# Kernel optimization log

Measured on AMD Instinct MI355X. Metric: run time of the kernel, lower is better.

The kernel has to match this reference:

```python
import jax, jax.numpy as jnp
import numpy as np

N_NODES = 50000
N_EDGES = 800000
N_GRAPHS = 64
D_IN = 96
D_HID = 96
D_OUT = 2
NEG_SLOPE = 0.2


def setup_inputs() -> dict:
    key = jax.random.key(0)
    ks = jax.random.split(key, 9)
    x = jax.random.normal(ks[0], (N_NODES, D_IN), dtype=jnp.float32)
    edge_index = jax.random.randint(ks[1], (2, N_EDGES), 0, N_NODES, dtype=jnp.int32)
    batch = jnp.sort(jax.random.randint(ks[2], (N_NODES,), 0, N_GRAPHS, dtype=jnp.int32))
    s1 = 1.0 / np.sqrt(D_IN)
    s2 = 1.0 / np.sqrt(D_HID)
    W1 = jax.random.normal(ks[3], (D_IN, D_HID), dtype=jnp.float32) * s1
    b1 = jnp.zeros((D_HID,), dtype=jnp.float32)
    W2 = jax.random.normal(ks[4], (D_HID, D_HID), dtype=jnp.float32) * s2
    b2 = jnp.zeros((D_HID,), dtype=jnp.float32)
    Wc = jax.random.normal(ks[5], (D_HID, D_OUT), dtype=jnp.float32) * s2
    bc = jnp.zeros((D_OUT,), dtype=jnp.float32)
    return {"x": x, "edge_index": edge_index, "batch": batch,
            "W1": W1, "b1": b1, "W2": W2, "b2": b2, "Wc": Wc, "bc": bc}


def _gcn_conv(h, W, b, src, dst, n_nodes):
    # GCNConv (Kipf): add self-loops, symmetric deg^-1/2 normalization.
    hW = h @ W  # [N, F]
    deg = jnp.zeros((n_nodes,), dtype=hW.dtype).at[dst].add(1.0) + 1.0  # +1 self-loop
    dinv = jax.lax.rsqrt(deg)
    coef = (dinv[src] * dinv[dst])[:, None]            # [E, 1]
    agg = jnp.zeros_like(hW).at[dst].add(hW[src] * coef)
    out = agg + hW * (dinv * dinv)[:, None] + b        # self-loop term: deg^-1 * hW
    return out


def _leaky(h):
    return jnp.where(h > 0, h, NEG_SLOPE * h)


def reference(x, edge_index, batch, W1, b1, W2, b2, Wc, bc):
    src, dst = edge_index[0], edge_index[1]
    h = _leaky(_gcn_conv(x, W1, b1, src, dst, N_NODES))
    h = _leaky(_gcn_conv(h, W2, b2, src, dst, N_NODES))
    # global_mean_pool over graph ids
    sums = jax.ops.segment_sum(h, batch, num_segments=N_GRAPHS)
    cnts = jax.ops.segment_sum(jnp.ones((N_NODES,), dtype=h.dtype), batch, num_segments=N_GRAPHS)
    pooled = sums / jnp.maximum(cnts, 1.0)[:, None]    # [G, F]
    return pooled @ Wc + bc                             # [G, D_OUT]
```

## Files before the change

### kernel.cpp

```cpp
#include <hip/hip_runtime.h>
#include <hip/hip_fp16.h>

#define NN 50000
#define NE 800000
#define NG 64
#define DF 96
#define SLOPE 0.2f
#define NBK 196
#define EB 196
#define PC 12

__global__ __launch_bounds__(256) void k_hist(const int* __restrict__ dst,
                                              int* __restrict__ hist2d) {
  __shared__ int h[NBK];
  int t = threadIdx.x;
  if (t < NBK) h[t] = 0;
  __syncthreads();
  int base = blockIdx.x * 4096;
  for (int k = 0; k < 16; ++k) {
    int e = base + k * 256 + t;
    if (e < NE) atomicAdd(&h[dst[e] >> 8], 1);
  }
  __syncthreads();
  if (t < NBK) hist2d[blockIdx.x * NBK + t] = h[t];
}

__global__ __launch_bounds__(256) void k_colscan(const int* __restrict__ hist2d,
                                                 int* __restrict__ colpref,
                                                 int* __restrict__ coltotal,
                                                 const int* __restrict__ batch,
                                                 int* __restrict__ gstart) {
  __shared__ int s[256];
  int col = blockIdx.x;
  int b = threadIdx.x;
  int v = (b < EB) ? hist2d[b * NBK + col] : 0;
  s[b] = v;
  __syncthreads();
  for (int o = 1; o < 256; o <<= 1) {
    int u = (b >= o) ? s[b - o] : 0;
    __syncthreads();
    s[b] += u;
    __syncthreads();
  }
  if (b < EB) colpref[b * NBK + col] = s[b] - v;
  if (b == 255) coltotal[col] = s[b];
  if (blockIdx.x == 0 && b <= NG) {
    int g = b, lo = 0, hi = NN;
    while (lo < hi) {
      int mid = (lo + hi) >> 1;
      if (batch[mid] < g) lo = mid + 1; else hi = mid;
    }
    gstart[g] = lo;
  }
}

__global__ __launch_bounds__(256) void k_bin2(const int* __restrict__ src,
                                              const int* __restrict__ dst,
                                              const int* __restrict__ hist2d,
                                              const int* __restrict__ coltotal,
                                              const int* __restrict__ colpref,
                                              int* __restrict__ binned) {
  __shared__ int h[NBK], loff[NBK], cur[NBK], gb[NBK];
  __shared__ int tmp[256];
  __shared__ int stage[4096];
  __shared__ unsigned char sbk[4096];
  int t = threadIdx.x;
  int ctv = (t < NBK) ? coltotal[t] : 0;
  tmp[t] = ctv;
  __syncthreads();
  for (int o = 1; o < 256; o <<= 1) {
    int u = (t >= o) ? tmp[t - o] : 0;
    __syncthreads();
    tmp[t] += u;
    __syncthreads();
  }
  int bbase_t = tmp[t] - ctv;
  if (t < NBK) h[t] = hist2d[blockIdx.x * NBK + t];
  __syncthreads();
  tmp[t] = (t < NBK) ? h[t] : 0;
  __syncthreads();
  for (int o = 1; o < 256; o <<= 1) {
    int u = (t >= o) ? tmp[t - o] : 0;
    __syncthreads();
    tmp[t] += u;
    __syncthreads();
  }
  if (t < NBK) {
    int excl = tmp[t] - h[t];
    loff[t] = excl;
    cur[t] = excl;
    gb[t] = bbase_t + colpref[blockIdx.x * NBK + t];
  }
  __syncthreads();
  int base = blockIdx.x * 4096;
  for (int k = 0; k < 16; ++k) {
    int e = base + k * 256 + t;
    if (e < NE) {
      int d = dst[e];
      int b = d >> 8;
      int p = atomicAdd(&cur[b], 1);
      stage[p] = src[e] | ((d & 255) << 16);
      sbk[p] = (unsigned char)b;
    }
  }
  __syncthreads();
  int tot = min(4096, NE - base);
  for (int i = t; i < tot; i += 256) {
    int b = sbk[i];
    binned[gb[b] + (i - loff[b])] = stage[i];
  }
}

__global__ __launch_bounds__(256) void k_csr(const int* __restrict__ binned,
                                             const int* __restrict__ coltotal,
                                             float* __restrict__ dinv,
                                             int* __restrict__ row_start,
                                             unsigned short* __restrict__ csr_src) {
  __shared__ int h[256], cur[256], tmp[256];
  int t = threadIdx.x;
  int b = blockIdx.x;
  int ctv = (t < NBK) ? coltotal[t] : 0;
  h[t] = ctv;
  tmp[t] = ctv;
  __syncthreads();
  for (int o = 1; o < 256; o <<= 1) {
    int u = (t >= o) ? tmp[t - o] : 0;
    __syncthreads();
    tmp[t] += u;
    __syncthreads();
  }
  int ebeg = tmp[b] - h[b];
  int eend = tmp[b];
  __syncthreads();
  h[t] = 0;
  __syncthreads();
  for (int i = ebeg + t; i < eend; i += 256) atomicAdd(&h[(unsigned)binned[i] >> 16], 1);
  __syncthreads();
  tmp[t] = h[t];
  __syncthreads();
  for (int o = 1; o < 256; o <<= 1) {
    int v = (t >= o) ? tmp[t - o] : 0;
    __syncthreads();
    tmp[t] += v;
    __syncthreads();
  }
  int excl = tmp[t] - h[t];
  int rs = ebeg + excl;
  cur[t] = rs;
  int n = b * 256 + t;
  if (n < NN) {
    row_start[n] = rs;
    dinv[n] = rsqrtf((float)h[t] + 1.0f);
  }
  if (b == NBK - 1 && t == 255) row_start[NN] = NE;
  __syncthreads();
  for (int i = ebeg + t; i < eend; i += 256) {
    int pr = binned[i];
    int p = atomicAdd(&cur[(unsigned)pr >> 16], 1);
    csr_src[p] = (unsigned short)(pr & 0xFFFF);
  }
}

#define GR 64
template <typename T>
__global__ __launch_bounds__(256) void k_gemm(const T* __restrict__ X,
                                              const float* __restrict__ W,
                                              const float* __restrict__ dinv,
                                              __half* __restrict__ G) {
  __shared__ float Ws[DF * DF];
  int t = threadIdx.x;
  for (int i = t; i < DF * DF / 4; i += 256)
    ((float4*)Ws)[i] = ((const float4*)W)[i];
  __syncthreads();
  int tc = t & 15;
  int tr = t >> 4;
  int c0 = tc * 6;
  int r0 = blockIdx.x * GR + tr * 4;
  const T* xp[4];
#pragma unroll
  for (int i = 0; i < 4; ++i) xp[i] = X + (size_t)min(r0 + i, NN - 1) * DF;

  float acc[4][6];
#pragma unroll
  for (int i = 0; i < 4; ++i)
#pragma unroll
    for (int j = 0; j < 6; ++j) acc[i][j] = 0.f;

#pragma unroll 4
  for (int k4 = 0; k4 < DF / 4; ++k4) {
    float xr[4][4];
#pragma unroll
    for (int i = 0; i < 4; ++i) {
      if constexpr (sizeof(T) == 4) {
        float4 v = ((const float4*)xp[i])[k4];
        xr[i][0] = v.x; xr[i][1] = v.y; xr[i][2] = v.z; xr[i][3] = v.w;
      } else {
        uint2 hv = ((const uint2*)xp[i])[k4];
        float2 a = __half22float2(*(__half2*)&hv.x);
        float2 b = __half22float2(*(__half2*)&hv.y);
        xr[i][0] = a.x; xr[i][1] = a.y; xr[i][2] = b.x; xr[i][3] = b.y;
      }
    }
#pragma unroll
    for (int kk = 0; kk < 4; ++kk) {
      int k = k4 * 4 + kk;
      float2 w0 = *(float2*)&Ws[k * DF + c0];
      float2 w1 = *(float2*)&Ws[k * DF + c0 + 2];
      float2 w2 = *(float2*)&Ws[k * DF + c0 + 4];
      float wv[6] = {w0.x, w0.y, w1.x, w1.y, w2.x, w2.y};
#pragma unroll
      for (int i = 0; i < 4; ++i)
#pragma unroll
        for (int j = 0; j < 6; ++j) acc[i][j] = fmaf(xr[i][kk], wv[j], acc[i][j]);
    }
  }
#pragma unroll
  for (int i = 0; i < 4; ++i) {
    int row = r0 + i;
    if (row < NN) {
      float dv = dinv[row];
      __half2* gp = (__half2*)(G + (size_t)row * DF + c0);
#pragma unroll
      for (int j = 0; j < 3; ++j)
        gp[j] = __floats2half2_rn(acc[i][2 * j] * dv, acc[i][2 * j + 1] * dv);
    }
  }
}

__global__ __launch_bounds__(256) void k_agg(const __half* __restrict__ G,
                                             const float* __restrict__ dinv,
                                             const float* __restrict__ bias,
                                             const int* __restrict__ row_start,
                                             const unsigned short* __restrict__ csr_src,
                                             __half* __restrict__ H) {
  int lane = threadIdx.x & 15;
  int n = blockIdx.x * 16 + (threadIdx.x >> 4);
  if (n >= NN) return;
  const unsigned* rn = (const unsigned*)(G + (size_t)n * DF);
  unsigned su0 = rn[lane], su1 = rn[lane + 16], su2 = rn[lane + 32];
  float2 f0 = __half22float2(*(__half2*)&su0);
  float2 f1 = __half22float2(*(__half2*)&su1);
  float2 f2 = __half22float2(*(__half2*)&su2);
  float a00 = f0.x, a01 = f0.y, a10 = f1.x, a11 = f1.y, a20 = f2.x, a21 = f2.y;

  int s = row_start[n], e = row_start[n + 1];
  for (int j0 = s; j0 < e; j0 += 16) {
    int my = (j0 + lane < e) ? (int)csr_src[j0 + lane] : 0;
    int cnt = min(16, e - j0);
    int jj = 0;
    for (; jj + 8 <= cnt; jj += 8) {
      unsigned u[8][3];
#pragma unroll
      for (int q = 0; q < 8; ++q) {
        int srcn = __shfl(my, jj + q, 16);
        const unsigned* r2 = (const unsigned*)(G + (size_t)srcn * DF);
        u[q][0] = r2[lane];
        u[q][1] = r2[lane + 16];
        u[q][2] = r2[lane + 32];
      }
#pragma unroll
      for (int q = 0; q < 8; ++q) {
        float2 g0 = __half22float2(*(__half2*)&u[q][0]);
        float2 g1 = __half22float2(*(__half2*)&u[q][1]);
        float2 g2 = __half22float2(*(__half2*)&u[q][2]);
        a00 += g0.x; a01 += g0.y;
        a10 += g1.x; a11 += g1.y;
        a20 += g2.x; a21 += g2.y;
      }
    }
    for (; jj < cnt; ++jj) {
      int srcn = __shfl(my, jj, 16);
      const unsigned* r2 = (const unsigned*)(G + (size_t)srcn * DF);
      unsigned v0 = r2[lane], v1 = r2[lane + 16], v2 = r2[lane + 32];
      float2 g0 = __half22float2(*(__half2*)&v0);
      float2 g1 = __half22float2(*(__half2*)&v1);
      float2 g2 = __half22float2(*(__half2*)&v2);
      a00 += g0.x; a01 += g0.y;
      a10 += g1.x; a11 += g1.y;
      a20 += g2.x; a21 += g2.y;
    }
  }
  float dv = dinv[n];
  float2 b0 = *(const float2*)(bias + 2 * lane);
  float2 b1 = *(const float2*)(bias + 2 * lane + 32);
  float2 b2 = *(const float2*)(bias + 2 * lane + 64);
  float v00 = dv * a00 + b0.x, v01 = dv * a01 + b0.y;
  float v10 = dv * a10 + b1.x, v11 = dv * a11 + b1.y;
  float v20 = dv * a20 + b2.x, v21 = dv * a21 + b2.y;
  v00 = v00 > 0.f ? v00 : SLOPE * v00;
  v01 = v01 > 0.f ? v01 : SLOPE * v01;
  v10 = v10 > 0.f ? v10 : SLOPE * v10;
  v11 = v11 > 0.f ? v11 : SLOPE * v11;
  v20 = v20 > 0.f ? v20 : SLOPE * v20;
  v21 = v21 > 0.f ? v21 : SLOPE * v21;
  __half2* hp = (__half2*)(H + (size_t)n * DF);
  hp[lane] = __floats2half2_rn(v00, v01);
  hp[lane + 16] = __floats2half2_rn(v10, v11);
  hp[lane + 32] = __floats2half2_rn(v20, v21);
}

__global__ __launch_bounds__(384) void k_pool2(const __half* __restrict__ H,
                                               const int* __restrict__ gstart,
                                               float* __restrict__ partial) {
  int g = blockIdx.x / PC, c = blockIdx.x % PC;
  int f2 = threadIdx.x % 48;
  int r = threadIdx.x / 48;
  int s = gstart[g], e = gstart[g + 1];
  int len = (e - s + PC - 1) / PC;
  int cs = s + c * len, ce = min(cs + len, e);
  float ax = 0.f, ay = 0.f;
  for (int n = cs + r; n < ce; n += 8) {
    float2 v = __half22float2(((const __half2*)(H + (size_t)n * DF))[f2]);
    ax += v.x;
    ay += v.y;
  }
  __shared__ float2 red[8][48];
  red[r][f2] = float2{ax, ay};
  __syncthreads();
  if (r == 0) {
    float sx = 0.f, sy = 0.f;
#pragma unroll
    for (int q = 0; q < 8; ++q) { sx += red[q][f2].x; sy += red[q][f2].y; }
    partial[(size_t)blockIdx.x * DF + 2 * f2] = sx;
    partial[(size_t)blockIdx.x * DF + 2 * f2 + 1] = sy;
  }
}

__global__ __launch_bounds__(128) void k_pool3(const float* __restrict__ partial,
                                               const int* __restrict__ gstart,
                                               const float* __restrict__ Wc,
                                               const float* __restrict__ bc,
                                               float* __restrict__ out) {
  __shared__ float pm[DF];
  int g = blockIdx.x;
  int t = threadIdx.x;
  if (t < DF) {
    float s = 0.f;
    for (int c = 0; c < PC; ++c) s += partial[(size_t)(g * PC + c) * DF + t];
    float cnt = (float)(gstart[g + 1] - gstart[g]);
    pm[t] = s / fmaxf(cnt, 1.0f);
  }
  __syncthreads();
  if (t < 2) {
    float s = 0.f;
    for (int c = 0; c < DF; ++c) s += pm[c] * Wc[c * 2 + t];
    out[g * 2 + t] = s + bc[t];
  }
}

extern "C" void kernel_launch(void* const* d_in, const int* in_sizes, int n_in,
                              void* d_out, int out_size, void* d_ws, size_t ws_size,
                              hipStream_t stream) {
  const float* x = (const float*)d_in[0];
  const int* ei = (const int*)d_in[1];
  const int* batch = (const int*)d_in[2];
  const float* W1 = (const float*)d_in[3];
  const float* b1 = (const float*)d_in[4];
  const float* W2 = (const float*)d_in[5];
  const float* b2 = (const float*)d_in[6];
  const float* Wc = (const float*)d_in[7];
  const float* bc = (const float*)d_in[8];
  float* out = (float*)d_out;
  const int* srcv = ei;
  const int* dstv = ei + NE;

  char* p = (char*)d_ws;
  auto alloc = [&](size_t bytes) {
    char* r = p;
    p += (bytes + 255) & ~(size_t)255;
    return r;
  };
  int* hist2d = (int*)alloc((size_t)EB * NBK * sizeof(int));
  int* colpref = (int*)alloc((size_t)EB * NBK * sizeof(int));
  int* coltotal = (int*)alloc((size_t)NBK * sizeof(int));
  int* gstart = (int*)alloc((size_t)(NG + 1) * sizeof(int));
  int* row_start = (int*)alloc((size_t)(NN + 1) * sizeof(int));
  int* binned = (int*)alloc((size_t)NE * sizeof(int));
  unsigned short* csr_src = (unsigned short*)alloc((size_t)NE * sizeof(unsigned short));
  float* dinv = (float*)alloc((size_t)NN * sizeof(float));
  __half* g = (__half*)alloc((size_t)NN * DF * sizeof(__half));
  __half* h = (__half*)alloc((size_t)NN * DF * sizeof(__half));
  float* partial = (float*)alloc((size_t)NG * PC * DF * sizeof(float));

  k_hist<<<EB, 256, 0, stream>>>(dstv, hist2d);
  k_colscan<<<NBK, 256, 0, stream>>>(hist2d, colpref, coltotal, batch, gstart);
  k_bin2<<<EB, 256, 0, stream>>>(srcv, dstv, hist2d, coltotal, colpref, binned);
  k_csr<<<NBK, 256, 0, stream>>>(binned, coltotal, dinv, row_start, csr_src);

  k_gemm<float><<<(NN + GR - 1) / GR, 256, 0, stream>>>(x, W1, dinv, g);
  k_agg<<<NN / 16, 256, 0, stream>>>(g, dinv, b1, row_start, csr_src, h);
  k_gemm<__half><<<(NN + GR - 1) / GR, 256, 0, stream>>>(h, W2, dinv, g);
  k_agg<<<NN / 16, 256, 0, stream>>>(g, dinv, b2, row_start, csr_src, h);

  k_pool2<<<NG * PC, 384, 0, stream>>>(h, gstart, partial);
  k_pool3<<<NG, 128, 0, stream>>>(partial, gstart, Wc, bc, out);
}
```

Before: 147.8 us.

## Sort nodes by degree for aggregation and use 12-byte vector row loads

Builds a degree histogram in the CSR kernel and adds a counting-sort kernel that produces a permutation of nodes ordered by in-degree. The aggregation kernel walks nodes in that order, so the 16-lane groups sharing a wavefront get similar neighbor counts and diverge less. It also changes each lane to own six contiguous features and fetch them with one 12-byte load instead of three strided 4-byte loads. The cost is an extra kernel launch plus atomics, the perm indirection, and less locality in destination-row writes.

```diff
diff --git a/kernel.cpp b/kernel.cpp
--- a/kernel.cpp
+++ b/kernel.cpp
@@ -29,7 +29,9 @@
                                                  int* __restrict__ colpref,
                                                  int* __restrict__ coltotal,
                                                  const int* __restrict__ batch,
-                                                 int* __restrict__ gstart) {
+                                                 int* __restrict__ gstart,
+                                                 int* __restrict__ deghist,
+                                                 int* __restrict__ classcnt) {
   __shared__ int s[256];
   int col = blockIdx.x;
   int b = threadIdx.x;
@@ -44,13 +46,17 @@
   }
   if (b < EB) colpref[b * NBK + col] = s[b] - v;
   if (b == 255) coltotal[col] = s[b];
-  if (blockIdx.x == 0 && b <= NG) {
-    int g = b, lo = 0, hi = NN;
-    while (lo < hi) {
-      int mid = (lo + hi) >> 1;
-      if (batch[mid] < g) lo = mid + 1; else hi = mid;
-    }
-    gstart[g] = lo;
+  if (blockIdx.x == 0) {
+    deghist[b] = 0;
+    classcnt[b] = 0;
+    if (b <= NG) {
+      int g = b, lo = 0, hi = NN;
+      while (lo < hi) {
+        int mid = (lo + hi) >> 1;
+        if (batch[mid] < g) lo = mid + 1; else hi = mid;
+      }
+      gstart[g] = lo;
+    }
   }
 }
 
@@ -115,8 +121,10 @@
                                              const int* __restrict__ coltotal,
                                              float* __restrict__ dinv,
                                              int* __restrict__ row_start,
-                                             unsigned short* __restrict__ csr_src) {
-  __shared__ int h[256], cur[256], tmp[256];
+                                             unsigned short* __restrict__ csr_src,
+                                             unsigned char* __restrict__ deg8,
+                                             int* __restrict__ deghist) {
+  __shared__ int h[256], cur[256], tmp[256], dh[256];
   int t = threadIdx.x;
   int b = blockIdx.x;
   int ctv = (t < NBK) ? coltotal[t] : 0;
@@ -133,6 +141,7 @@
   int eend = tmp[b];
   __syncthreads();
   h[t] = 0;
+  dh[t] = 0;
   __syncthreads();
   for (int i = ebeg + t; i < eend; i += 256) atomicAdd(&h[(unsigned)binned[i] >> 16], 1);
   __syncthreads();
@@ -144,20 +153,50 @@
     tmp[t] += v;
     __syncthreads();
   }
-  int excl = tmp[t] - h[t];
-  int rs = ebeg + excl;
+  int mydeg = h[t];
+  int rs = ebeg + (tmp[t] - mydeg);
   cur[t] = rs;
   int n = b * 256 + t;
   if (n < NN) {
     row_start[n] = rs;
-    dinv[n] = rsqrtf((float)h[t] + 1.0f);
+    dinv[n] = rsqrtf((float)mydeg + 1.0f);
+    int c = min(mydeg, 255);
+    deg8[n] = (unsigned char)c;
+    atomicAdd(&dh[c], 1);
   }
   if (b == NBK - 1 && t == 255) row_start[NN] = NE;
   __syncthreads();
+  if (dh[t]) atomicAdd(&deghist[t], dh[t]);
   for (int i = ebeg + t; i < eend; i += 256) {
     int pr = binned[i];
     int p = atomicAdd(&cur[(unsigned)pr >> 16], 1);
     csr_src[p] = (unsigned short)(pr & 0xFFFF);
+  }
+}
+
+__global__ __launch_bounds__(256) void k_perm(const unsigned char* __restrict__ deg8,
+                                              const int* __restrict__ deghist,
+                                              int* __restrict__ classcnt,
+                                              int* __restrict__ perm) {
+  __shared__ int s[256];
+  __shared__ int base[256];
+  int t = threadIdx.x;
+  int v = deghist[t];
+  s[t] = v;
+  __syncthreads();
+  for (int o = 1; o < 256; o <<= 1) {
+    int u = (t >= o) ? s[t - o] : 0;
+    __syncthreads();
+    s[t] += u;
+    __syncthreads();
+  }
+  base[t] = s[t] - v;
+  __syncthreads();
+  int n = blockIdx.x * 256 + t;
+  if (n < NN) {
+    int c = deg8[n];
+    int p = base[c] + atomicAdd(&classcnt[c], 1);
+    perm[p] = n;
   }
 }
 
@@ -232,16 +271,16 @@
                                              const float* __restrict__ bias,
                                              const int* __restrict__ row_start,
                                              const unsigned short* __restrict__ csr_src,
+                                             const int* __restrict__ perm,
                                              __half* __restrict__ H) {
   int lane = threadIdx.x & 15;
-  int n = blockIdx.x * 16 + (threadIdx.x >> 4);
-  if (n >= NN) return;
-  const unsigned* rn = (const unsigned*)(G + (size_t)n * DF);
-  unsigned su0 = rn[lane], su1 = rn[lane + 16], su2 = rn[lane + 32];
-  float2 f0 = __half22float2(*(__half2*)&su0);
-  float2 f1 = __half22float2(*(__half2*)&su1);
-  float2 f2 = __half22float2(*(__half2*)&su2);
-  float a00 = f0.x, a01 = f0.y, a10 = f1.x, a11 = f1.y, a20 = f2.x, a21 = f2.y;
+  int n = perm[blockIdx.x * 16 + (threadIdx.x >> 4)];
+  const char* Gb = (const char*)G;
+  uint3 sv = *(const uint3*)(Gb + (size_t)n * 192 + lane * 12);
+  float2 f0 = __half22float2(*(__half2*)&sv.x);
+  float2 f1 = __half22float2(*(__half2*)&sv.y);
+  float2 f2 = __half22float2(*(__half2*)&sv.z);
+  float a0 = f0.x, a1 = f0.y, a2 = f1.x, a3 = f1.y, a4 = f2.x, a5 = f2.y;
 
   int s = row_start[n], e = row_start[n + 1];
   for (int j0 = s; j0 < e; j0 += 16) {
@@ -249,54 +288,44 @@
     int cnt = min(16, e - j0);
     int jj = 0;
     for (; jj + 8 <= cnt; jj += 8) {
-      unsigned u[8][3];
+      uint3 u[8];
+#pragma unroll
+      for (int q = 0; q < 8; ++q)
+        u[q] = *(const uint3*)(Gb + (size_t)__shfl(my, jj + q, 16) * 192 + lane * 12);
 #pragma unroll
       for (int q = 0; q < 8; ++q) {
-        int srcn = __shfl(my, jj + q, 16);
-        const unsigned* r2 = (const unsigned*)(G + (size_t)srcn * DF);
-        u[q][0] = r2[lane];
-        u[q][1] = r2[lane + 16];
-        u[q][2] = r2[lane + 32];
+        float2 g0 = __half22float2(*(__half2*)&u[q].x);
+        float2 g1 = __half22float2(*(__half2*)&u[q].y);
+        float2 g2 = __half22float2(*(__half2*)&u[q].z);
+        a0 += g0.x; a1 += g0.y; a2 += g1.x; a3 += g1.y; a4 += g2.x; a5 += g2.y;
       }
-#pragma unroll
-      for (int q = 0; q < 8; ++q) {
-        float2 g0 = __half22float2(*(__half2*)&u[q][0]);
-        float2 g1 = __half22float2(*(__half2*)&u[q][1]);
-        float2 g2 = __half22float2(*(__half2*)&u[q][2]);
-        a00 += g0.x; a01 += g0.y;
-        a10 += g1.x; a11 += g1.y;
-        a20 += g2.x; a21 += g2.y;
-      }
     }
     for (; jj < cnt; ++jj) {
-      int srcn = __shfl(my, jj, 16);
-      const unsigned* r2 = (const unsigned*)(G + (size_t)srcn * DF);
-      unsigned v0 = r2[lane], v1 = r2[lane + 16], v2 = r2[lane + 32];
-      float2 g0 = __half22float2(*(__half2*)&v0);
-      float2 g1 = __half22float2(*(__half2*)&v1);
-      float2 g2 = __half22float2(*(__half2*)&v2);
-      a00 += g0.x; a01 += g0.y;
-      a10 += g1.x; a11 += g1.y;
-      a20 += g2.x; a21 += g2.y;
+      uint3 u = *(const uint3*)(Gb + (size_t)__shfl(my, jj, 16) * 192 + lane * 12);
+      float2 g0 = __half22float2(*(__half2*)&u.x);
+      float2 g1 = __half22float2(*(__half2*)&u.y);
+      float2 g2 = __half22float2(*(__half2*)&u.z);
+      a0 += g0.x; a1 += g0.y; a2 += g1.x; a3 += g1.y; a4 += g2.x; a5 += g2.y;
     }
   }
   float dv = dinv[n];
-  float2 b0 = *(const float2*)(bias + 2 * lane);
-  float2 b1 = *(const float2*)(bias + 2 * lane + 32);
-  float2 b2 = *(const float2*)(bias + 2 * lane + 64);
-  float v00 = dv * a00 + b0.x, v01 = dv * a01 + b0.y;
-  float v10 = dv * a10 + b1.x, v11 = dv * a11 + b1.y;
-  float v20 = dv * a20 + b2.x, v21 = dv * a21 + b2.y;
-  v00 = v00 > 0.f ? v00 : SLOPE * v00;
-  v01 = v01 > 0.f ? v01 : SLOPE * v01;
-  v10 = v10 > 0.f ? v10 : SLOPE * v10;
-  v11 = v11 > 0.f ? v11 : SLOPE * v11;
-  v20 = v20 > 0.f ? v20 : SLOPE * v20;
-  v21 = v21 > 0.f ? v21 : SLOPE * v21;
-  __half2* hp = (__half2*)(H + (size_t)n * DF);
-  hp[lane] = __floats2half2_rn(v00, v01);
-  hp[lane + 16] = __floats2half2_rn(v10, v11);
-  hp[lane + 32] = __floats2half2_rn(v20, v21);
+  float2 b0 = *(const float2*)(bias + 6 * lane);
+  float2 b1 = *(const float2*)(bias + 6 * lane + 2);
+  float2 b2 = *(const float2*)(bias + 6 * lane + 4);
+  float v0 = dv * a0 + b0.x, v1 = dv * a1 + b0.y;
+  float v2 = dv * a2 + b1.x, v3 = dv * a3 + b1.y;
+  float v4 = dv * a4 + b2.x, v5 = dv * a5 + b2.y;
+  v0 = v0 > 0.f ? v0 : SLOPE * v0;
+  v1 = v1 > 0.f ? v1 : SLOPE * v1;
+  v2 = v2 > 0.f ? v2 : SLOPE * v2;
+  v3 = v3 > 0.f ? v3 : SLOPE * v3;
+  v4 = v4 > 0.f ? v4 : SLOPE * v4;
+  v5 = v5 > 0.f ? v5 : SLOPE * v5;
+  uint3 o;
+  *(__half2*)&o.x = __floats2half2_rn(v0, v1);
+  *(__half2*)&o.y = __floats2half2_rn(v2, v3);
+  *(__half2*)&o.z = __floats2half2_rn(v4, v5);
+  *(uint3*)((char*)H + (size_t)n * 192 + lane * 12) = o;
 }
 
 __global__ __launch_bounds__(384) void k_pool2(const __half* __restrict__ H,
@@ -378,19 +407,24 @@
   int* binned = (int*)alloc((size_t)NE * sizeof(int));
   unsigned short* csr_src = (unsigned short*)alloc((size_t)NE * sizeof(unsigned short));
   float* dinv = (float*)alloc((size_t)NN * sizeof(float));
+  unsigned char* deg8 = (unsigned char*)alloc((size_t)NN);
+  int* deghist = (int*)alloc(256 * sizeof(int));
+  int* classcnt = (int*)alloc(256 * sizeof(int));
+  int* perm = (int*)alloc((size_t)NN * sizeof(int));
   __half* g = (__half*)alloc((size_t)NN * DF * sizeof(__half));
   __half* h = (__half*)alloc((size_t)NN * DF * sizeof(__half));
   float* partial = (float*)alloc((size_t)NG * PC * DF * sizeof(float));
 
   k_hist<<<EB, 256, 0, stream>>>(dstv, hist2d);
-  k_colscan<<<NBK, 256, 0, stream>>>(hist2d, colpref, coltotal, batch, gstart);
+  k_colscan<<<NBK, 256, 0, stream>>>(hist2d, colpref, coltotal, batch, gstart, deghist, classcnt);
   k_bin2<<<EB, 256, 0, stream>>>(srcv, dstv, hist2d, coltotal, colpref, binned);
-  k_csr<<<NBK, 256, 0, stream>>>(binned, coltotal, dinv, row_start, csr_src);
+  k_csr<<<NBK, 256, 0, stream>>>(binned, coltotal, dinv, row_start, csr_src, deg8, deghist);
+  k_perm<<<NBK, 256, 0, stream>>>(deg8, deghist, classcnt, perm);
 
   k_gemm<float><<<(NN + GR - 1) / GR, 256, 0, stream>>>(x, W1, dinv, g);
-  k_agg<<<NN / 16, 256, 0, stream>>>(g, dinv, b1, row_start, csr_src, h);
+  k_agg<<<NN / 16, 256, 0, stream>>>(g, dinv, b1, row_start, csr_src, perm, h);
   k_gemm<__half><<<(NN + GR - 1) / GR, 256, 0, stream>>>(h, W2, dinv, g);
-  k_agg<<<NN / 16, 256, 0, stream>>>(g, dinv, b2, row_start, csr_src, h);
+  k_agg<<<NN / 16, 256, 0, stream>>>(g, dinv, b2, row_start, csr_src, perm, h);
 
   k_pool2<<<NG * PC, 384, 0, stream>>>(h, gstart, partial);
   k_pool3<<<NG, 128, 0, stream>>>(partial, gstart, Wc, bc, out);
```

After: 283.1 us. 91.6% more time.

## Use MFMA f16 matrix cores for the dense feature transform GEMMs

Applied to the files above, without the earlier changes.

Replaces the scalar FMA register-tiled GEMM with a version built on the 16x16x32 f16 MFMA instruction. The weight matrix is converted to fp16 and stored transposed in padded shared memory, and the input rows are loaded as half8 fragments. The goal is to cut ALU time in the two X@W steps. In exchange the first layer's fp32 input and both weight matrices are now quantized to fp16 before multiplication, and the output stores become scattered 2-byte writes.

```diff
diff --git a/kernel.cpp b/kernel.cpp
--- a/kernel.cpp
+++ b/kernel.cpp
@@ -9,6 +9,9 @@
 #define NBK 196
 #define EB 196
 #define PC 12
+
+using half8 = __attribute__((ext_vector_type(8))) _Float16;
+using f32x4 = __attribute__((ext_vector_type(4))) float;
 
 __global__ __launch_bounds__(256) void k_hist(const int* __restrict__ dst,
                                               int* __restrict__ hist2d) {
@@ -161,68 +164,63 @@
   }
 }
 
-#define GR 64
+#define WTP 104
 template <typename T>
 __global__ __launch_bounds__(256) void k_gemm(const T* __restrict__ X,
                                               const float* __restrict__ W,
                                               const float* __restrict__ dinv,
                                               __half* __restrict__ G) {
-  __shared__ float Ws[DF * DF];
-  int t = threadIdx.x;
-  for (int i = t; i < DF * DF / 4; i += 256)
-    ((float4*)Ws)[i] = ((const float4*)W)[i];
-  __syncthreads();
-  int tc = t & 15;
-  int tr = t >> 4;
-  int c0 = tc * 6;
-  int r0 = blockIdx.x * GR + tr * 4;
-  const T* xp[4];
-#pragma unroll
-  for (int i = 0; i < 4; ++i) xp[i] = X + (size_t)min(r0 + i, NN - 1) * DF;
-
-  float acc[4][6];
-#pragma unroll
-  for (int i = 0; i < 4; ++i)
-#pragma unroll
-    for (int j = 0; j < 6; ++j) acc[i][j] = 0.f;
-
-#pragma unroll 4
-  for (int k4 = 0; k4 < DF / 4; ++k4) {
-    float xr[4][4];
-#pragma unroll
-    for (int i = 0; i < 4; ++i) {
-      if constexpr (sizeof(T) == 4) {
-        float4 v = ((const float4*)xp[i])[k4];
-        xr[i][0] = v.x; xr[i][1] = v.y; xr[i][2] = v.z; xr[i][3] = v.w;
-      } else {
-        uint2 hv = ((const uint2*)xp[i])[k4];
-        float2 a = __half22float2(*(__half2*)&hv.x);
-        float2 b = __half22float2(*(__half2*)&hv.y);
-        xr[i][0] = a.x; xr[i][1] = a.y; xr[i][2] = b.x; xr[i][3] = b.y;
-      }
-    }
-#pragma unroll
-    for (int kk = 0; kk < 4; ++kk) {
-      int k = k4 * 4 + kk;
-      float2 w0 = *(float2*)&Ws[k * DF + c0];
-      float2 w1 = *(float2*)&Ws[k * DF + c0 + 2];
-      float2 w2 = *(float2*)&Ws[k * DF + c0 + 4];
-      float wv[6] = {w0.x, w0.y, w1.x, w1.y, w2.x, w2.y};
-#pragma unroll
-      for (int i = 0; i < 4; ++i)
-#pragma unroll
-        for (int j = 0; j < 6; ++j) acc[i][j] = fmaf(xr[i][kk], wv[j], acc[i][j]);
-    }
-  }
-#pragma unroll
-  for (int i = 0; i < 4; ++i) {
-    int row = r0 + i;
-    if (row < NN) {
-      float dv = dinv[row];
-      __half2* gp = (__half2*)(G + (size_t)row * DF + c0);
-#pragma unroll
-      for (int j = 0; j < 3; ++j)
-        gp[j] = __floats2half2_rn(acc[i][2 * j] * dv, acc[i][2 * j + 1] * dv);
+  __shared__ alignas(16) _Float16 Wt[DF * WTP];
+  int t = threadIdx.x;
+  for (int i = t; i < DF * DF; i += 256) {
+    int k = i / DF, c = i % DF;
+    Wt[c * WTP + k] = (_Float16)W[i];
+  }
+  __syncthreads();
+
+  int wave = t >> 6;
+  int lane = t & 63;
+  int lrow = lane & 15;
+  int kgrp = lane >> 4;
+  int rowbase = blockIdx.x * 64 + wave * 16;
+  int arow = min(rowbase + lrow, NN - 1);
+
+  half8 a[3];
+#pragma unroll
+  for (int kt = 0; kt < 3; ++kt) {
+    int k0 = kt * 32 + kgrp * 8;
+    if constexpr (sizeof(T) == 4) {
+      const float4* xp = (const float4*)((const float*)X + (size_t)arow * DF + k0);
+      float4 v0 = xp[0], v1 = xp[1];
+      a[kt][0] = (_Float16)v0.x; a[kt][1] = (_Float16)v0.y;
+      a[kt][2] = (_Float16)v0.z; a[kt][3] = (_Float16)v0.w;
+      a[kt][4] = (_Float16)v1.x; a[kt][5] = (_Float16)v1.y;
+      a[kt][6] = (_Float16)v1.z; a[kt][7] = (_Float16)v1.w;
+    } else {
+      a[kt] = *(const half8*)((const _Float16*)X + (size_t)arow * DF + k0);
+    }
+  }
+
+  float dvv[4];
+  int orow0 = rowbase + kgrp * 4;
+#pragma unroll
+  for (int r = 0; r < 4; ++r)
+    dvv[r] = (orow0 + r < NN) ? dinv[orow0 + r] : 0.f;
+
+#pragma unroll
+  for (int ct = 0; ct < 6; ++ct) {
+    int colbase = ct * 16;
+    f32x4 acc = {0.f, 0.f, 0.f, 0.f};
+#pragma unroll
+    for (int kt = 0; kt < 3; ++kt) {
+      half8 b = *(const half8*)&Wt[(colbase + lrow) * WTP + kt * 32 + kgrp * 8];
+      acc = __builtin_amdgcn_mfma_f32_16x16x32_f16(a[kt], b, acc, 0, 0, 0);
+    }
+#pragma unroll
+    for (int r = 0; r < 4; ++r) {
+      int orow = orow0 + r;
+      if (orow < NN)
+        G[(size_t)orow * DF + colbase + lrow] = __float2half(acc[r] * dvv[r]);
     }
   }
 }
@@ -387,10 +385,11 @@
   k_bin2<<<EB, 256, 0, stream>>>(srcv, dstv, hist2d, coltotal, colpref, binned);
   k_csr<<<NBK, 256, 0, stream>>>(binned, coltotal, dinv, row_start, csr_src);
 
-  k_gemm<float><<<(NN + GR - 1) / GR, 256, 0, stream>>>(x, W1, dinv, g);
-  k_agg<<<NN / 16, 256, 0, stream>>>(g, dinv, b1, row_start, csr_src, h);
-  k_gemm<__half><<<(NN + GR - 1) / GR, 256, 0, stream>>>(h, W2, dinv, g);
-  k_agg<<<NN / 16, 256, 0, stream>>>(g, dinv, b2, row_start, csr_src, h);
+  const int GB = (NN + 63) / 64;
+  k_gemm<float><<<GB, 256, 0, stream>>>(x, W1, dinv, g);
+  k_agg<<<(NN + 15) / 16, 256, 0, stream>>>(g, dinv, b1, row_start, csr_src, h);
+  k_gemm<__half><<<GB, 256, 0, stream>>>((const __half*)h, W2, dinv, g);
+  k_agg<<<(NN + 15) / 16, 256, 0, stream>>>(g, dinv, b2, row_start, csr_src, h);
 
   k_pool2<<<NG * PC, 384, 0, stream>>>(h, gstart, partial);
   k_pool3<<<NG, 128, 0, stream>>>(partial, gstart, Wc, bc, out);
```

Result: faster. 126.1 us (-14.7%).
